# Kernel optimization log

Measured on AMD Instinct MI355X. Metric: run time of the kernel, lower is better.

## Reference

```python
import jax, jax.numpy as jnp
import numpy as np

B, S, D_IN, D_H = 8, 2048, 512, 512

def setup_inputs() -> dict:
    key = jax.random.key(0)
    ks = jax.random.split(key, 7)
    s = 1.0 / np.sqrt(D_IN)
    return {
        "x": jax.random.normal(ks[0], (B, S, D_IN), dtype=jnp.float32),
        "Wq": jax.random.uniform(ks[1], (D_H, D_IN), jnp.float32, -s, s),
        "bq": jax.random.uniform(ks[2], (D_H,), jnp.float32, -s, s),
        "Wk": jax.random.uniform(ks[3], (D_H, D_IN), jnp.float32, -s, s),
        "bk": jax.random.uniform(ks[4], (D_H,), jnp.float32, -s, s),
        "Wv": jax.random.uniform(ks[5], (D_H, D_IN), jnp.float32, -s, s),
        "bv": jax.random.uniform(ks[6], (D_H,), jnp.float32, -s, s),
    }

def reference(x, Wq, bq, Wk, bk, Wv, bv):
    # torch Linear: y = x @ W.T + b
    Q = jnp.einsum('bsd,hd->bsh', x, Wq) + bq
    K = jnp.einsum('bsd,hd->bsh', x, Wk) + bk
    V = jnp.einsum('bsd,hd->bsh', x, Wv) + bv
    scale = jnp.sqrt(jnp.asarray(D_H, dtype=x.dtype))
    scores = jnp.einsum('bqh,bkh->bqk', Q, K) / scale  # [B,S,S]
    attn = jax.nn.softmax(scores, axis=-1)
    return jnp.einsum('bqk,bkh->bqh', attn, V)
```

## Files before the change

kernel.cpp:

```cpp
#include <hip/hip_runtime.h>
#include <hip/hip_bf16.h>
#include <cstdint>

#define B_   8
#define S_   2048
#define DIN  512
#define DH   512

typedef __attribute__((ext_vector_type(8))) short  short8;
typedef __attribute__((ext_vector_type(4))) short  short4_;
typedef __attribute__((ext_vector_type(4))) float  float4_;

__device__ inline unsigned short f2bf(float f) {
    union { float f; unsigned u; } v; v.f = f;
    unsigned u = v.u;
    u += 0x7fffu + ((u >> 16) & 1u);
    return (unsigned short)(u >> 16);
}

__device__ inline void gload_lds16(const void* g, void* l) {
    __builtin_amdgcn_global_load_lds(
        (const __attribute__((address_space(1))) void*)g,
        (__attribute__((address_space(3))) void*)l, 16, 0, 0);
}

__device__ inline void barrier_lds_only() {
    __asm__ volatile("s_waitcnt lgkmcnt(0)\n\ts_barrier" ::: "memory");
}

__global__ __launch_bounds__(256) void conv_bf16(
    const float* __restrict__ x,
    const float* __restrict__ Wq, const float* __restrict__ Wk, const float* __restrict__ Wv,
    unsigned short* __restrict__ xb, unsigned short* __restrict__ wb)
{
    const int NX4 = (B_ * S_ * DIN) / 4;
    const int NW4 = (DH * DIN) / 4;
    const int total = NX4 + 3 * NW4;
    for (int i = blockIdx.x * blockDim.x + threadIdx.x; i < total;
         i += gridDim.x * blockDim.x) {
        const float4_* src; unsigned short* dst; int j;
        if (i < NX4)             { src = (const float4_*)x;  dst = xb;            j = i; }
        else if (i < NX4 + NW4)  { src = (const float4_*)Wq; dst = wb;            j = i - NX4; }
        else if (i < NX4 + 2*NW4){ src = (const float4_*)Wk; dst = wb + DH*DIN;   j = i - NX4 - NW4; }
        else                     { src = (const float4_*)Wv; dst = wb + 2*DH*DIN; j = i - NX4 - 2*NW4; }
        float4_ v = src[j];
        short4_ o;
        o[0] = (short)f2bf(v[0]); o[1] = (short)f2bf(v[1]);
        o[2] = (short)f2bf(v[2]); o[3] = (short)f2bf(v[3]);
        ((short4_*)dst)[j] = o;
    }
}

__global__ __launch_bounds__(256) void qkv_gemm(
    const unsigned short* __restrict__ xb,
    const unsigned short* __restrict__ wb,
    const float* __restrict__ bq, const float* __restrict__ bk, const float* __restrict__ bv,
    unsigned short* __restrict__ qws, unsigned short* __restrict__ kws,
    unsigned short* __restrict__ vt2)
{
    __shared__ __align__(16) unsigned short smem[17408];

    const int tm   = blockIdx.x;
    const int tc   = blockIdx.y;
    const int mat  = tc >> 2;
    const int nb   = (tc & 3) * 128;
    const int tid  = threadIdx.x;
    const int w    = tid >> 6;
    const int lane = tid & 63;
    const int l15  = lane & 15;
    const int quad = lane >> 4;
    const int wm   = (w & 1) * 64;
    const int wn   = (w >> 1) * 64;
    const int m0   = tm * 128;

    const unsigned short* wmat = wb + (size_t)mat * DH * DIN;

    float4_ zero = {0.f, 0.f, 0.f, 0.f};
    float4_ acc[4][4];
    #pragma unroll
    for (int i = 0; i < 4; i++)
        #pragma unroll
        for (int j = 0; j < 4; j++) acc[i][j] = zero;

    const int lr = lane >> 2;
    const int lb = (lane & 3) * 16;

    auto stage = [&](int kk, int bufi) {
        unsigned short* Ab = smem + bufi * 8192;
        unsigned short* Bb = smem + 4096 + bufi * 8192;
        #pragma unroll
        for (int c = 0; c < 2; c++) {
            int r = w * 32 + c * 16;
            const unsigned char* gA = (const unsigned char*)(xb + (size_t)(m0 + r) * DIN + kk);
            gload_lds16(gA + (size_t)lr * (DIN * 2) + lb, (void*)(Ab + r * 32));
            const unsigned char* gB = (const unsigned char*)(wmat + (size_t)(nb + r) * DIN + kk);
            gload_lds16(gB + (size_t)lr * (DIN * 2) + lb, (void*)(Bb + r * 32));
        }
    };

    stage(0, 0);
    for (int ki = 0; ki < 16; ki++) {
        __syncthreads();
        if (ki < 15) stage((ki + 1) * 32, (ki + 1) & 1);
        const unsigned short* Ab = smem + (ki & 1) * 8192;
        const unsigned short* Bb = smem + 4096 + (ki & 1) * 8192;
        short8 af[4], bf[4];
        #pragma unroll
        for (int mt = 0; mt < 4; mt++)
            af[mt] = *(const short8*)(Ab + (wm + mt * 16 + l15) * 32 + quad * 8);
        #pragma unroll
        for (int nt = 0; nt < 4; nt++)
            bf[nt] = *(const short8*)(Bb + (wn + nt * 16 + l15) * 32 + quad * 8);
        #pragma unroll
        for (int mt = 0; mt < 4; mt++)
            #pragma unroll
            for (int nt = 0; nt < 4; nt++)
                acc[mt][nt] = __builtin_amdgcn_mfma_f32_16x16x32_bf16(af[mt], bf[nt], acc[mt][nt], 0, 0, 0);
    }

    if (mat < 2) {
        const float* bias  = (mat == 0) ? bq : bk;
        const float  scale = (mat == 0) ? 0.044194173824159216f : 1.0f;
        unsigned short* dst = (mat == 0) ? qws : kws;
        #pragma unroll
        for (int nt = 0; nt < 4; nt++) {
            int n = nb + wn + nt * 16 + l15;
            float bv_ = bias[n];
            #pragma unroll
            for (int mt = 0; mt < 4; mt++) {
                #pragma unroll
                for (int r = 0; r < 4; r++) {
                    int m = m0 + wm + mt * 16 + quad * 4 + r;
                    dst[(size_t)m * DH + n] = f2bf((acc[mt][nt][r] + bv_) * scale);
                }
            }
        }
    } else {
        __syncthreads();
        unsigned short* trans = smem;
        #pragma unroll
        for (int nt = 0; nt < 4; nt++) {
            int dloc = wn + nt * 16 + l15;
            float bv_ = bv[nb + dloc];
            #pragma unroll
            for (int mt = 0; mt < 4; mt++) {
                short4_ pk;
                #pragma unroll
                for (int r = 0; r < 4; r++) pk[r] = (short)f2bf(acc[mt][nt][r] + bv_);
                *(short4_*)(trans + dloc * 136 + wm + mt * 16 + quad * 4) = pk;
            }
        }
        __syncthreads();
        int dl   = tid >> 1;
        int h    = tid & 1;
        int dh_g = nb + dl;
        int s4   = (dh_g >> 2) & 3;
        int bi   = m0 >> 11;
        int tile0 = (m0 & 2047) >> 4;
        unsigned char* vt2b = (unsigned char*)vt2;
        #pragma unroll
        for (int t = 0; t < 4; t++) {
            int tl = h * 4 + t;
            const uint2* c = (const uint2*)(trans + dl * 136 + tl * 16);
            uint2 d0 = c[0 ^ s4], d1 = c[1 ^ s4], d2 = c[2 ^ s4], d3 = c[3 ^ s4];
            unsigned char* dst = vt2b + ((size_t)(bi * 128 + tile0 + tl) << 14) + dh_g * 32;
            ((uint2*)dst)[0] = d0; ((uint2*)dst)[1] = d1;
            ((uint2*)dst)[2] = d2; ((uint2*)dst)[3] = d3;
        }
    }
}

__global__ __launch_bounds__(512, 2) void attn(
    const unsigned short* __restrict__ qws,
    const unsigned short* __restrict__ kws,
    const unsigned short* __restrict__ vt2,
    float* __restrict__ out)
{
    __shared__ __align__(16) unsigned char smem[141824];

    const int bid  = blockIdx.x;
    const int b    = bid & 7;
    const int qt_b = bid >> 3;
    const int tid  = threadIdx.x;
    const int w    = tid >> 6;
    const int g    = w >> 2;
    const int wl   = w & 3;
    const int lane = tid & 63;
    const int l15  = lane & 15;
    const int quad = lane >> 4;

    const int qrow0  = b * S_ + qt_b * 64;
    const int myqrow = qrow0 + wl * 16;

    const unsigned short* kgrp = kws + (size_t)(b * S_ + g * 1024) * DH;
    const unsigned char*  vtb  = (const unsigned char*)vt2;

    unsigned char*  kb  = smem + g * 65536;
    unsigned char*  vb  = smem + g * 65536 + 32768;
    unsigned short* pg  = (unsigned short*)(smem + 136192 + g * 2560);
    float*          lbuf= (float*)(smem + 141312);

    short8 qf[16];
    {
        const short8* qp = (const short8*)(qws + (size_t)(myqrow + l15) * DH);
        #pragma unroll
        for (int ksi = 0; ksi < 16; ksi++) qf[ksi] = qp[ksi * 4 + quad];
    }

    float4_ zero = {0.f, 0.f, 0.f, 0.f};
    float4_ o[32];
    #pragma unroll
    for (int i = 0; i < 32; i++) o[i] = zero;
    float4_ ol[4];
    #pragma unroll
    for (int i = 0; i < 4; i++) ol[i] = zero;

    short4_ ones;
    ones[0] = ones[1] = ones[2] = ones[3] = (short)0x3F80;

    auto stageK = [&](int n, int bufi) {
        #pragma unroll
        for (int i = 0; i < 4; i++) {
            int row = wl * 4 + i;
            const unsigned char* gp =
                (const unsigned char*)(kgrp + (size_t)(n * 16 + row) * DH);
            gload_lds16(gp + ((lane ^ (row & 7)) << 4),
                        kb + bufi * 16384 + row * 1024);
        }
    };
    auto stageV = [&](int n, int bufi) {
        const unsigned char* base =
            vtb + ((size_t)(b * 128 + g * 64 + n) << 14) + wl * 4096;
        #pragma unroll
        for (int i = 0; i < 4; i++)
            gload_lds16(base + i * 1024 + lane * 16,
                        vb + bufi * 16384 + wl * 4096 + i * 1024);
    };

    stageK(0, 0); stageV(0, 0);
    int cur = 0;

    for (int it = 0; it < 64; it++) {
        __syncthreads();

        if (it < 63) { stageK(it + 1, cur ^ 1); stageV(it + 1, cur ^ 1); }

        const unsigned char* kt_ = kb + cur * 16384;
        float4_ s0 = zero, s1 = zero;
        #pragma unroll
        for (int ksi = 0; ksi < 16; ksi += 2) {
            short8 k0 = *(const short8*)(kt_ + l15 * 1024 + ((( ksi      * 4 + quad) ^ (l15 & 7)) << 4));
            short8 k1 = *(const short8*)(kt_ + l15 * 1024 + ((((ksi + 1) * 4 + quad) ^ (l15 & 7)) << 4));
            s0 = __builtin_amdgcn_mfma_f32_16x16x32_bf16(qf[ksi],     k0, s0, 0, 0, 0);
            s1 = __builtin_amdgcn_mfma_f32_16x16x32_bf16(qf[ksi + 1], k1, s1, 0, 0, 0);
        }
        float4_ sc = s0 + s1;

        #pragma unroll
        for (int r = 0; r < 4; r++)
            pg[(wl * 16 + quad * 4 + r) * 20 + l15] = f2bf(__expf(sc[r]));

        barrier_lds_only();

        {
            const unsigned char* vt_ = vb + cur * 16384;
            short4_ pa[4];
            #pragma unroll
            for (int qt = 0; qt < 4; qt++)
                pa[qt] = *(const short4_*)((const unsigned char*)pg + (qt * 16 + l15) * 40 + quad * 8);
            #pragma unroll
            for (int qt = 0; qt < 4; qt++)
                ol[qt] = __builtin_amdgcn_mfma_f32_16x16x16bf16_1k(pa[qt], ones, ol[qt], 0, 0, 0);
            #pragma unroll
            for (int dht = 0; dht < 8; dht++) {
                int dh_sl = wl * 128 + dht * 16 + l15;
                short4_ vf = *(const short4_*)(vt_ + dh_sl * 32 + ((quad ^ ((dh_sl >> 2) & 3)) << 3));
                #pragma unroll
                for (int qt = 0; qt < 4; qt++)
                    o[qt * 8 + dht] = __builtin_amdgcn_mfma_f32_16x16x16bf16_1k(pa[qt], vf, o[qt * 8 + dht], 0, 0, 0);
            }
        }
        cur ^= 1;
    }

    if (wl == 0 && l15 == 0) {
        #pragma unroll
        for (int qt = 0; qt < 4; qt++)
            #pragma unroll
            for (int r = 0; r < 4; r++)
                lbuf[g * 64 + qt * 16 + quad * 4 + r] = ol[qt][r];
    }
    __syncthreads();
    if (g == 1) {
        float* om = (float*)(smem + wl * 33280);
        #pragma unroll
        for (int qt = 0; qt < 4; qt++)
            #pragma unroll
            for (int dht = 0; dht < 8; dht++)
                #pragma unroll
                for (int r = 0; r < 4; r++)
                    om[(qt * 16 + quad * 4 + r) * 130 + dht * 16 + l15] = o[qt * 8 + dht][r];
    }
    __syncthreads();
    if (g == 0) {
        const float* om = (const float*)(smem + wl * 33280);
        #pragma unroll
        for (int qt = 0; qt < 4; qt++) {
            float rl[4];
            #pragma unroll
            for (int r = 0; r < 4; r++) {
                int row = qt * 16 + quad * 4 + r;
                rl[r] = 1.f / (lbuf[row] + lbuf[64 + row]);
            }
            #pragma unroll
            for (int dht = 0; dht < 8; dht++)
                #pragma unroll
                for (int r = 0; r < 4; r++) {
                    int row = qt * 16 + quad * 4 + r;
                    out[(size_t)(qrow0 + row) * DH + wl * 128 + dht * 16 + l15] =
                        (o[qt * 8 + dht][r] + om[row * 130 + dht * 16 + l15]) * rl[r];
                }
        }
    }
}

extern "C" void kernel_launch(void* const* d_in, const int* in_sizes, int n_in,
                              void* d_out, int out_size, void* d_ws, size_t ws_size,
                              hipStream_t stream) {
    const float* x  = (const float*)d_in[0];
    const float* Wq = (const float*)d_in[1];
    const float* bq = (const float*)d_in[2];
    const float* bk = (const float*)d_in[4];
    const float* Wk = (const float*)d_in[3];
    const float* Wv = (const float*)d_in[5];
    const float* bv = (const float*)d_in[6];
    float* out = (float*)d_out;

    unsigned short* qws = (unsigned short*)d_ws;
    unsigned short* kws = qws + (size_t)B_ * S_ * DH;
    unsigned short* vt2 = kws + (size_t)B_ * S_ * DH;

    unsigned short* xb = (unsigned short*)d_out;
    unsigned short* wb = xb + (size_t)B_ * S_ * DIN;

    conv_bf16<<<dim3(2048), dim3(256), 0, stream>>>(x, Wq, Wk, Wv, xb, wb);
    qkv_gemm<<<dim3(128, 12), dim3(256), 0, stream>>>(xb, wb, bq, bk, bv, qws, kws, vt2);
    attn<<<dim3(256), dim3(512), 0, stream>>>(qws, kws, vt2, out);
}
```

Measured before the change: 302.3 us.

## Software-pipeline attention loop: overlap QK of this tile with PV of previous

```diff
diff --git a/kernel.cpp b/kernel.cpp
--- a/kernel.cpp
+++ b/kernel.cpp
@@ -22,10 +22,6 @@
     __builtin_amdgcn_global_load_lds(
         (const __attribute__((address_space(1))) void*)g,
         (__attribute__((address_space(3))) void*)l, 16, 0, 0);
-}
-
-__device__ inline void barrier_lds_only() {
-    __asm__ volatile("s_waitcnt lgkmcnt(0)\n\ts_barrier" ::: "memory");
 }
 
 __global__ __launch_bounds__(256) void conv_bf16(
@@ -195,10 +191,10 @@
     const unsigned short* kgrp = kws + (size_t)(b * S_ + g * 1024) * DH;
     const unsigned char*  vtb  = (const unsigned char*)vt2;
 
-    unsigned char*  kb  = smem + g * 65536;
-    unsigned char*  vb  = smem + g * 65536 + 32768;
-    unsigned short* pg  = (unsigned short*)(smem + 136192 + g * 2560);
-    float*          lbuf= (float*)(smem + 141312);
+    unsigned char* kb    = smem + g * 65536;
+    unsigned char* vb    = smem + g * 65536 + 32768;
+    unsigned char* pbase = smem + 131072 + g * 5120;
+    float*         lbuf  = (float*)(smem + 141312);
 
     short8 qf[16];
     {
@@ -237,15 +233,35 @@
                         vb + bufi * 16384 + wl * 4096 + i * 1024);
     };
 
-    stageK(0, 0); stageV(0, 0);
-    int cur = 0;
+    auto doPV = [&](int bufi) {
+        const unsigned char* vt_ = vb + bufi * 16384;
+        const unsigned char* pp  = pbase + bufi * 2560;
+        short4_ pa[4];
+        #pragma unroll
+        for (int qt = 0; qt < 4; qt++)
+            pa[qt] = *(const short4_*)(pp + (qt * 16 + l15) * 40 + quad * 8);
+        #pragma unroll
+        for (int qt = 0; qt < 4; qt++)
+            ol[qt] = __builtin_amdgcn_mfma_f32_16x16x16bf16_1k(pa[qt], ones, ol[qt], 0, 0, 0);
+        #pragma unroll
+        for (int dht = 0; dht < 8; dht++) {
+            int dh_sl = wl * 128 + dht * 16 + l15;
+            short4_ vf = *(const short4_*)(vt_ + dh_sl * 32 + ((quad ^ ((dh_sl >> 2) & 3)) << 3));
+            #pragma unroll
+            for (int qt = 0; qt < 4; qt++)
+                o[qt * 8 + dht] = __builtin_amdgcn_mfma_f32_16x16x16bf16_1k(pa[qt], vf, o[qt * 8 + dht], 0, 0, 0);
+        }
+    };
+
+    stageK(0, 0);
 
     for (int it = 0; it < 64; it++) {
         __syncthreads();
 
-        if (it < 63) { stageK(it + 1, cur ^ 1); stageV(it + 1, cur ^ 1); }
-
-        const unsigned char* kt_ = kb + cur * 16384;
+        if (it < 63) stageK(it + 1, (it + 1) & 1);
+        stageV(it, it & 1);
+
+        const unsigned char* kt_ = kb + (it & 1) * 16384;
         float4_ s0 = zero, s1 = zero;
         #pragma unroll
         for (int ksi = 0; ksi < 16; ksi += 2) {
@@ -256,32 +272,16 @@
         }
         float4_ sc = s0 + s1;
 
+        unsigned short* pp = (unsigned short*)(pbase + (it & 1) * 2560);
         #pragma unroll
         for (int r = 0; r < 4; r++)
-            pg[(wl * 16 + quad * 4 + r) * 20 + l15] = f2bf(__expf(sc[r]));
-
-        barrier_lds_only();
-
-        {
-            const unsigned char* vt_ = vb + cur * 16384;
-            short4_ pa[4];
-            #pragma unroll
-            for (int qt = 0; qt < 4; qt++)
-                pa[qt] = *(const short4_*)((const unsigned char*)pg + (qt * 16 + l15) * 40 + quad * 8);
-            #pragma unroll
-            for (int qt = 0; qt < 4; qt++)
-                ol[qt] = __builtin_amdgcn_mfma_f32_16x16x16bf16_1k(pa[qt], ones, ol[qt], 0, 0, 0);
-            #pragma unroll
-            for (int dht = 0; dht < 8; dht++) {
-                int dh_sl = wl * 128 + dht * 16 + l15;
-                short4_ vf = *(const short4_*)(vt_ + dh_sl * 32 + ((quad ^ ((dh_sl >> 2) & 3)) << 3));
-                #pragma unroll
-                for (int qt = 0; qt < 4; qt++)
-                    o[qt * 8 + dht] = __builtin_amdgcn_mfma_f32_16x16x16bf16_1k(pa[qt], vf, o[qt * 8 + dht], 0, 0, 0);
-            }
-        }
-        cur ^= 1;
-    }
+            pp[(wl * 16 + quad * 4 + r) * 20 + l15] = f2bf(__expf(sc[r]));
+
+        if (it) doPV((it - 1) & 1);
+    }
+
+    __syncthreads();
+    doPV(1);
 
     if (wl == 0 && l15 == 0) {
         #pragma unroll
@@ -330,8 +330,8 @@
     const float* x  = (const float*)d_in[0];
     const float* Wq = (const float*)d_in[1];
     const float* bq = (const float*)d_in[2];
+    const float* Wk = (const float*)d_in[3];
     const float* bk = (const float*)d_in[4];
-    const float* Wk = (const float*)d_in[3];
     const float* Wv = (const float*)d_in[5];
     const float* bv = (const float*)d_in[6];
     float* out = (float*)d_out;
```

New measurement: 279.9 us. 7.4% less time.
